# Optimization experiments

Hardware: AMD Instinct MI355X
Metric: run time of the kernel (lower is better)

## Reference

```python
import jax, jax.numpy as jnp
import numpy as np


def setup_inputs() -> dict:
    key = jax.random.key(0)
    ks = jax.random.split(key, 8)
    B, S, P = 512, 128, 32            # batch, seq_len, pred_len
    F, O, H = 64, 64, 1024            # feat_dim, label/output_dim, hidden_dim
    IN = F + O                        # GRUCell input_dim = 128
    w = 0.05                          # weight scale to keep gates in useful range
    return {
        "feats": jax.random.normal(ks[0], (B, S + P - 1, F), jnp.float32),
        "labels": jax.random.normal(ks[1], (B, S, O), jnp.float32),
        "Wi": jax.random.normal(ks[2], (3 * H, IN), jnp.float32) * w,
        "Wh": jax.random.normal(ks[3], (3 * H, H), jnp.float32) * w,
        "bi": jax.random.normal(ks[4], (3 * H,), jnp.float32) * w,
        "bh": jax.random.normal(ks[5], (3 * H,), jnp.float32) * w,
        "Wd": jax.random.normal(ks[6], (O, H), jnp.float32) * w,
        "bd": jax.random.normal(ks[7], (O,), jnp.float32) * w,
    }


def _gru_cell(h, x, Wi, Wh, bi, bh):
    # torch.nn.GRUCell semantics
    gi = x @ Wi.T + bi                       # [B, 3H]
    gh = h @ Wh.T + bh                       # [B, 3H]
    i_r, i_z, i_n = jnp.split(gi, 3, axis=-1)
    h_r, h_z, h_n = jnp.split(gh, 3, axis=-1)
    r = jax.nn.sigmoid(i_r + h_r)
    z = jax.nn.sigmoid(i_z + h_z)
    n = jnp.tanh(i_n + r * h_n)
    return (1.0 - z) * n + z * h


def reference(feats, labels, Wi, Wh, bi, bh, Wd, bd):
    B, S, O = labels.shape
    H = Wh.shape[1]
    prior = feats[:, :S]                     # [B, S, F]
    post = feats[:, S:]                      # [B, P-1, F]
    x = jnp.concatenate([prior, labels], axis=-1)   # [B, S, F+O]

    h0 = jnp.zeros((B, H), feats.dtype)

    def enc_step(h, xt):
        return _gru_cell(h, xt, Wi, Wh, bi, bh), None

    h, _ = jax.lax.scan(enc_step, h0, jnp.swapaxes(x, 0, 1))

    ps = h @ Wd.T + bd                       # decoder output [B, O]

    def dec_step(carry, ft):
        h, ps = carry
        xin = jnp.concatenate([ft, ps], axis=-1)
        h = _gru_cell(h, xin, Wi, Wh, bi, bh)
        ps = h @ Wd.T + bd
        return (h, ps), ps

    _, rest = jax.lax.scan(dec_step, (h, ps), jnp.swapaxes(post, 0, 1))
    return jnp.concatenate([ps[None], rest], axis=0)  # [pred_len, B, O]
```

## Files before the change

### kernel.cpp

```cpp
#include <hip/hip_runtime.h>
#include <cstdint>
#include <cstddef>

#define SENC  128
#define NSTEPS 159
#define HB16  524288
#define XSLICE 131072
#define SLAB_ELEMS 55296
#define FRAG_TOTAL 442368
#define FS 16

typedef short  short8  __attribute__((ext_vector_type(8)));
typedef float  floatx4 __attribute__((ext_vector_type(4)));
typedef float  f32x4   __attribute__((ext_vector_type(4)));
typedef int    i32x4   __attribute__((ext_vector_type(4)));
typedef unsigned long long u64;

#define MFMA(a, b, c) __builtin_amdgcn_mfma_f32_16x16x32_bf16((a), (b), (c), 0, 0, 0)

__device__ __forceinline__ i32x4 ld_nc16(const void* p) {
    i32x4 r;
    asm volatile("global_load_dwordx4 %0, %1, off sc0 sc1" : "=&v"(r) : "v"(p) : "memory");
    return r;
}
__device__ __forceinline__ i32x4 ld_sc0_16(const void* p) {
    i32x4 r;
    asm volatile("global_load_dwordx4 %0, %1, off sc0" : "=&v"(r) : "v"(p) : "memory");
    return r;
}
__device__ __forceinline__ void st_nc8(void* p, u64 v) {
    asm volatile("global_store_dwordx2 %0, %1, off sc0 sc1" :: "v"(p), "v"(v) : "memory");
}
#define WAITVM(N) asm volatile("s_waitcnt vmcnt(" #N ")" ::: "memory")
#define WAITLGKM  asm volatile("s_waitcnt lgkmcnt(0)" ::: "memory")

__device__ __forceinline__ unsigned ldu_dev(const unsigned* p) {
    return __hip_atomic_load(p, __ATOMIC_RELAXED, __HIP_MEMORY_SCOPE_AGENT);
}
__device__ __forceinline__ u64 ldq_dev(const u64* p) {
    return __hip_atomic_load(p, __ATOMIC_RELAXED, __HIP_MEMORY_SCOPE_AGENT);
}
__device__ __forceinline__ void stu_dev(unsigned* p, unsigned v) {
    __hip_atomic_store(p, v, __ATOMIC_RELAXED, __HIP_MEMORY_SCOPE_AGENT);
}
__device__ __forceinline__ void stf_dev(float* p, float v) {
    __hip_atomic_store(p, v, __ATOMIC_RELAXED, __HIP_MEMORY_SCOPE_AGENT);
}

__device__ __forceinline__ unsigned ld_ws(const unsigned* p) {
    return __hip_atomic_load(p, __ATOMIC_RELAXED, __HIP_MEMORY_SCOPE_WORKGROUP);
}
__device__ __forceinline__ void st_ws(unsigned* p, unsigned v) {
    __hip_atomic_store(p, v, __ATOMIC_RELAXED, __HIP_MEMORY_SCOPE_WORKGROUP);
}
__device__ __forceinline__ unsigned add_ws(unsigned* p, unsigned v) {
    return __hip_atomic_fetch_add(p, v, __ATOMIC_RELAXED, __HIP_MEMORY_SCOPE_WORKGROUP);
}

__device__ __forceinline__ float bf2f(short s) {
    return __uint_as_float(((unsigned)(unsigned short)s) << 16);
}
__device__ __forceinline__ short f2bf(float f) {
    unsigned u = __float_as_uint(f);
    return (short)((u + 0x7FFFu + ((u >> 16) & 1u)) >> 16);
}
__device__ __forceinline__ void f2pair(float f, short& hi, short& lo) {
    hi = f2bf(f);
    lo = f2bf(f - bf2f(hi));
}

__device__ __forceinline__ float sigm(float x) {
    return 1.0f / (1.0f + __expf(-x));
}
__device__ __forceinline__ float tanh_fast(float x) {
    float cx = fminf(fmaxf(x, -15.0f), 15.0f);
    float e = __expf(2.0f * cx);
    return (e - 1.0f) / (e + 1.0f);
}

__global__ void setup_swizzle(const float* __restrict__ Wi, const float* __restrict__ Wh,
                              short* __restrict__ whi, short* __restrict__ wlo_x) {
    const int idx = blockIdx.x * 256 + threadIdx.x;
    if (idx >= FRAG_TOTAL) return;
    const int l    = idx & 63;
    const int rest = idx >> 6;
    const int t    = rest % 3;
    const int ki   = (rest / 3) % 36;
    const int c    = rest / 108;
    const int nrow = t * 1024 + c * 16 + (l & 15);
    const int kb   = ki * 32 + (l >> 4) * 8;
    short8 vh, vl;
#pragma unroll
    for (int j = 0; j < 8; ++j) {
        const int k = kb + j;
        float w = (k < 128) ? Wi[(size_t)nrow * 128 + k]
                            : Wh[(size_t)nrow * 1024 + (k - 128)];
        short h, lo2;
        f2pair(w, h, lo2);
        vh[j] = h; vl[j] = lo2;
    }
    *(short8*)(whi + (size_t)idx * 8) = vh;
    if (ki < 4) {
        const int xi = ((c * 4 + ki) * 3 + t) * 64 + l;
        *(short8*)(wlo_x + (size_t)xi * 8) = vl;
    }
}

#define HCONS(S, KI) do { \
    short8 ah_ = *(short8*)&hb[S]; \
    const int fo_ = (((KI) * 3) * 64 + lane) * 8; \
    short8 b0_ = *(const short8*)(s_whi + fo_); \
    short8 b1_ = *(const short8*)(s_whi + fo_ + 512); \
    short8 b2_ = *(const short8*)(s_whi + fo_ + 1024); \
    aR  = MFMA(ah_, b0_, aR); \
    aZ  = MFMA(ah_, b1_, aZ); \
    aNh = MFMA(ah_, b2_, aNh); \
} while (0)

#define IS4(LDFN, B, K0) do { \
    hb[(B) + 0] = LDFN(hrd + ((K0) - 4) * 4096); \
    hb[(B) + 1] = LDFN(hrd + ((K0) - 3) * 4096); \
    hb[(B) + 2] = LDFN(hrd + ((K0) - 2) * 4096); \
    hb[(B) + 3] = LDFN(hrd + ((K0) - 1) * 4096); \
} while (0)

#define CONS4(B, K0) do { \
    HCONS((B) + 0, (K0) + 0); \
    HCONS((B) + 1, (K0) + 1); \
    HCONS((B) + 2, (K0) + 2); \
    HCONS((B) + 3, (K0) + 3); \
} while (0)

#define SPINS(S) do { \
    while (ld_ws(&s_sub[S]) < (unsigned)step) __builtin_amdgcn_s_sleep(2); \
} while (0)

#define REGION2(LDFN) do { \
    i32x4 hb[16]; \
    SPINS(0); IS4(LDFN, 0, 4); \
    SPINS(1); IS4(LDFN, 4, 8); \
    SPINS(2); IS4(LDFN, 8, 12); \
    SPINS(3); IS4(LDFN, 12, 16); \
    WAITVM(12); CONS4(0, 4);   SPINS(4); IS4(LDFN, 0, 20); \
    WAITVM(12); CONS4(4, 8);   SPINS(5); IS4(LDFN, 4, 24); \
    WAITVM(12); CONS4(8, 12);  SPINS(6); IS4(LDFN, 8, 28); \
    WAITVM(12); CONS4(12, 16); SPINS(7); IS4(LDFN, 12, 32); \
    WAITVM(12); CONS4(0, 20); \
    WAITVM(8);  CONS4(4, 24); \
    WAITVM(4);  CONS4(8, 28); \
    WAITVM(0);  CONS4(12, 32); \
} while (0)

#define R1TRIPLE(KI) do { \
    short8 ah_, al_; \
    _Pragma("unroll") \
    for (int j = 0; j < 8; ++j) { short h2_, l2_; f2pair(f[j], h2_, l2_); ah_[j] = h2_; al_[j] = l2_; } \
    const int fo_ = (((KI) * 3) * 64 + lane) * 8; \
    short8 b0_ = *(const short8*)(s_whi + fo_); \
    short8 b1_ = *(const short8*)(s_whi + fo_ + 512); \
    short8 b2_ = *(const short8*)(s_whi + fo_ + 1024); \
    aR  = MFMA(ah_, b0_, aR);  aR  = MFMA(ah_, L0r[KI], aR);  aR  = MFMA(al_, b0_, aR); \
    aZ  = MFMA(ah_, b1_, aZ);  aZ  = MFMA(ah_, L1r[KI], aZ);  aZ  = MFMA(al_, b1_, aZ); \
    aNi = MFMA(ah_, b2_, aNi); aNi = MFMA(ah_, L2r[KI], aNi); aNi = MFMA(al_, b2_, aNi); \
} while (0)

#define LOADF(KI) do { \
    const float* s_ = feats + ((size_t)brow * 159 + step) * 64 + (KI) * 32 + q * 8; \
    f32x4 a_ = ((const f32x4*)s_)[0], b_ = ((const f32x4*)s_)[1]; \
    _Pragma("unroll") for (int j = 0; j < 4; ++j) { f[j] = a_[j]; f[4 + j] = b_[j]; } \
} while (0)

#define LOADL(KI) do { \
    const float* s_ = labels + ((size_t)brow * 128 + step) * 64 + ((KI) - 2) * 32 + q * 8; \
    f32x4 a_ = ((const f32x4*)s_)[0], b_ = ((const f32x4*)s_)[1]; \
    _Pragma("unroll") for (int j = 0; j < 4; ++j) { f[j] = a_[j]; f[4 + j] = b_[j]; } \
} while (0)

#define LOADP(KI) do { \
    const u64* pp_ = (const u64*)(ps_f32 + (size_t)brow * 64 + ((KI) - 2) * 32 + q * 8); \
    _Pragma("unroll") for (int j = 0; j < 4; ++j) { \
        u64 v_ = ldq_dev(pp_ + j); \
        f[2 * j]     = __uint_as_float((unsigned)v_); \
        f[2 * j + 1] = __uint_as_float((unsigned)(v_ >> 32)); } \
} while (0)

__global__ __launch_bounds__(512, 2) void gru_main(
    const float* __restrict__ feats, const float* __restrict__ labels,
    const float* __restrict__ bi,    const float* __restrict__ bh,
    const float* __restrict__ Wd,    const float* __restrict__ bd,
    const short* __restrict__ whi_sw, const short* __restrict__ wlo_x,
    short* __restrict__ h16,         float* __restrict__ ps_f32,
    float* __restrict__ out,
    unsigned* __restrict__ hflag,
    unsigned* __restrict__ pflag,
    int nslots)
{
    __shared__ short s_whi[SLAB_ELEMS];
    __shared__ float s_ps[2048];
    __shared__ short s_tr[8][16][18];
    __shared__ unsigned s_sub[8];
    __shared__ unsigned s_arrD, s_arrI;

    const int tid  = threadIdx.x;
    const int lane = tid & 63;
    const int wv   = tid >> 6;
    const int q    = lane >> 4;
    const int n16  = lane & 15;
    const int c    = blockIdx.x & 63;
    const int r    = blockIdx.x >> 6;
    const bool cached = (nslots > 2);

    if (tid < 8) s_sub[tid] = 0;
    if (tid == 8) s_arrD = 0;
    if (tid == 9) s_arrI = 0;
    {
        const f32x4* src = (const f32x4*)(whi_sw + (size_t)c * SLAB_ELEMS);
        f32x4* dst = (f32x4*)s_whi;
        for (int i = tid; i < SLAB_ELEMS / 8; i += 512) dst[i] = src[i];
    }
    __syncthreads();

    const int mbase = r * 128 + wv * 16;
    const int brow  = mbase + n16;
    const int row_r = c * 16 + n16;
    const float bias_r  = bi[row_r] + bh[row_r];
    const float bias_z  = bi[1024 + row_r] + bh[1024 + row_r];
    const float bias_ni = bi[2048 + row_r];
    const float bias_nh = bh[2048 + row_r];

    unsigned* my_hflag = hflag + (r * 64 + c) * FS;
    unsigned* my_pflag = pflag + (r * 64 + c) * FS;
    const unsigned* hfp     = hflag + (r * 64 + 8 * wv + (lane & 7)) * FS;
    const unsigned* grp_hfl = hflag + (r * 64) * FS;
    const unsigned* grp_pfl = pflag + (r * 64) * FS;

    short8 L0r[4], L1r[4], L2r[4];
#pragma unroll
    for (int ki = 0; ki < 4; ++ki) {
        const short* base = wlo_x + (size_t)(((c * 4 + ki) * 3) * 64 + lane) * 8;
        L0r[ki] = *(const short8*)(base);
        L1r[ki] = *(const short8*)(base + 512);
        L2r[ki] = *(const short8*)(base + 1024);
    }

    float hold[4] = {0.f, 0.f, 0.f, 0.f};

    for (int step = 0; step < NSTEPS; ++step) {
        const bool dec = (step >= SENC);
        const unsigned tgt = (unsigned)(step + 1);
        const int rslot = cached ? step       : (step & 1);
        const int wslot = cached ? (step + 1) : ((step + 1) & 1);
        const short* hrd = h16 + (size_t)rslot * HB16 + (size_t)r * XSLICE
                         + (size_t)(wv * 16 + n16) * 16 + (q & 1) * 8 + (q >> 1) * 2048;
        short* hwr = h16 + (size_t)wslot * HB16 + (size_t)r * XSLICE;

        floatx4 aR  = (floatx4){bias_r,  bias_r,  bias_r,  bias_r};
        floatx4 aZ  = (floatx4){bias_z,  bias_z,  bias_z,  bias_z};
        floatx4 aNi = (floatx4){bias_ni, bias_ni, bias_ni, bias_ni};
        floatx4 aNh = (floatx4){bias_nh, bias_nh, bias_nh, bias_nh};

        {
            float f[8];
            LOADF(0); R1TRIPLE(0);
            LOADF(1); R1TRIPLE(1);

            if (step > 0 && step <= SENC - 1) {
                WAITVM(0);
                if (lane == 0) {
                    unsigned old = add_ws(&s_arrD, 1u);
                    if (old == 8u * (unsigned)step - 1u)
                        stu_dev(my_hflag, (unsigned)step);
                }
            }

            if (!dec) {
                LOADL(2); R1TRIPLE(2);
                LOADL(3); R1TRIPLE(3);
            } else {
                if (wv == 0) {
                    while (ldu_dev(grp_pfl + lane * FS) < (unsigned)step)
                        __builtin_amdgcn_s_sleep(2);
                }
                __syncthreads();
                LOADP(2); R1TRIPLE(2);
                LOADP(3); R1TRIPLE(3);
            }
        }

        if (step > 0) {
            while (!__all(ldu_dev(hfp) >= (unsigned)step))
                __builtin_amdgcn_s_sleep(2);
            if (lane == 0) st_ws(&s_sub[wv], (unsigned)step);
            if (cached) { REGION2(ld_sc0_16); }
            else        { REGION2(ld_nc16); }
        }

        {
#pragma unroll
            for (int i = 0; i < 4; ++i) {
                float rr = sigm(aR[i]);
                float zz = sigm(aZ[i]);
                float nn = tanh_fast(aNi[i] + rr * aNh[i]);
                float hv = (1.0f - zz) * nn + zz * hold[i];
                hold[i] = hv;
                s_tr[wv][q * 4 + i][n16] = f2bf(hv);
            }
            WAITLGKM;
            const int rr2 = lane >> 2, seg = lane & 3;
            u64 v = *(const u64*)&s_tr[wv][rr2][seg * 4];
            st_nc8(hwr + (size_t)c * 2048 + (size_t)(wv * 16 + rr2) * 16 + seg * 4, v);
            if (step >= SENC - 1) {
                WAITVM(0);
                if (lane == 0) {
                    unsigned old = add_ws(&s_arrI, 1u);
                    if (old == 8u * (unsigned)(step - (SENC - 1) + 1) - 1u)
                        stu_dev(my_hflag, tgt);
                }
            }
        }

        if (step >= SENC - 1) {
            const int ot = step - (SENC - 1);
            const int prow0 = r * 128 + 2 * c;
            if (wv == 0) {
                while (ldu_dev(grp_hfl + lane * FS) < tgt)
                    __builtin_amdgcn_s_sleep(2);
            }
            __syncthreads();
            if (tid < 256) {
                const int rl = tid >> 7, rest = tid & 127;
                const int ct = rest >> 1, half = rest & 1;
                const short* src = hwr + (size_t)ct * 2048
                                 + (size_t)(2 * c + rl) * 16 + half * 8;
                i32x4 v = ld_nc16(src);
                WAITVM(0);
                short8 s = *(short8*)&v;
#pragma unroll
                for (int j = 0; j < 8; ++j)
                    s_ps[rl * 1024 + ct * 16 + half * 8 + j] = bf2f(s[j]);
            }
            __syncthreads();
            const int o = tid >> 3, e = tid & 7;
            const float* wrow = Wd + (size_t)o * 1024;
            float acc0 = 0.0f, acc1 = 0.0f;
#pragma unroll 8
            for (int j = 0; j < 32; ++j) {
                const int k = j * 32 + e * 4;
                f32x4 w  = *(const f32x4*)(wrow + k);
                f32x4 a4 = *(const f32x4*)(s_ps + k);
                f32x4 b4 = *(const f32x4*)(s_ps + 1024 + k);
                acc0 += a4[0] * w[0] + a4[1] * w[1] + a4[2] * w[2] + a4[3] * w[3];
                acc1 += b4[0] * w[0] + b4[1] * w[1] + b4[2] * w[2] + b4[3] * w[3];
            }
            acc0 += __shfl_xor(acc0, 1); acc0 += __shfl_xor(acc0, 2); acc0 += __shfl_xor(acc0, 4);
            acc1 += __shfl_xor(acc1, 1); acc1 += __shfl_xor(acc1, 2); acc1 += __shfl_xor(acc1, 4);
            if (e == 0) {
                float v0 = acc0 + bd[o];
                float v1 = acc1 + bd[o];
                out[((size_t)ot * 512 + prow0)     * 64 + o] = v0;
                out[((size_t)ot * 512 + prow0 + 1) * 64 + o] = v1;
                stf_dev(ps_f32 + (size_t)prow0       * 64 + o, v0);
                stf_dev(ps_f32 + (size_t)(prow0 + 1) * 64 + o, v1);
            }
            WAITVM(0);
            __syncthreads();
            if (tid == 0) stu_dev(my_pflag, tgt);
        }
    }
}

extern "C" void kernel_launch(void* const* d_in, const int* in_sizes, int n_in,
                              void* d_out, int out_size, void* d_ws, size_t ws_size,
                              hipStream_t stream) {
    const float* feats  = (const float*)d_in[0];
    const float* labels = (const float*)d_in[1];
    const float* Wi     = (const float*)d_in[2];
    const float* Wh     = (const float*)d_in[3];
    const float* bi     = (const float*)d_in[4];
    const float* bh     = (const float*)d_in[5];
    const float* Wd     = (const float*)d_in[6];
    const float* bd     = (const float*)d_in[7];
    float* out = (float*)d_out;

    char* ws = (char*)d_ws;
    short*    whi_sw = (short*)(ws);
    short*    wlo_x  = (short*)(ws + 7077888);
    float*    ps_f32 = (float*)(ws + 7864320);
    unsigned* pflag  = (unsigned*)(ws + 7995392);
    unsigned* hflag  = (unsigned*)(ws + 8011776);
    short*    h16    = (short*)(ws + 8388608);

    const size_t need = 8388608ull + 160ull * 1048576ull;
    int nslots = (ws_size >= need) ? 160 : 2;

    hipMemsetAsync(ws + 7995392, 0, 32768, stream);

    setup_swizzle<<<FRAG_TOTAL / 256, 256, 0, stream>>>(Wi, Wh, whi_sw, wlo_x);

    void* args[] = {(void*)&feats, (void*)&labels, (void*)&bi, (void*)&bh,
                    (void*)&Wd, (void*)&bd, (void*)&whi_sw, (void*)&wlo_x,
                    (void*)&h16, (void*)&ps_f32, (void*)&out,
                    (void*)&hflag, (void*)&pflag, (void*)&nslots};
    hipLaunchCooperativeKernel(reinterpret_cast<void*>(gru_main),
                               dim3(256), dim3(512), args, 0, stream);
}
```

Measured before the change: 1.483 ms.

## Stagger hidden-state chunk reads per block and publish via atomic swaps

Each block now starts its reads of the shared hidden-state chunks at an offset derived from its column index (c & 7) and wraps around, so that the 64 column blocks do not all spin on and load the same chunk at the same moment. Cross-block stores of the hidden state and the decoder output are changed from plain non-temporal stores and relaxed atomic stores to global atomic swap instructions. The swaps are meant to push the data to the device-coherent level sooner so that consumers polling on other blocks see it with less delay. They add atomic traffic, and the staggered order alters the per-chunk sub-flag wait pattern.

```diff
diff --git a/kernel.cpp b/kernel.cpp
--- a/kernel.cpp
+++ b/kernel.cpp
@@ -28,8 +28,11 @@
     asm volatile("global_load_dwordx4 %0, %1, off sc0" : "=&v"(r) : "v"(p) : "memory");
     return r;
 }
-__device__ __forceinline__ void st_nc8(void* p, u64 v) {
-    asm volatile("global_store_dwordx2 %0, %1, off sc0 sc1" :: "v"(p), "v"(v) : "memory");
+__device__ __forceinline__ void st_swap8(void* p, u64 v) {
+    asm volatile("global_atomic_swap_x2 %0, %1, off sc1" :: "v"(p), "v"(v) : "memory");
+}
+__device__ __forceinline__ void st_swap4(void* p, unsigned v) {
+    asm volatile("global_atomic_swap %0, %1, off sc1" :: "v"(p), "v"(v) : "memory");
 }
 #define WAITVM(N) asm volatile("s_waitcnt vmcnt(" #N ")" ::: "memory")
 #define WAITLGKM  asm volatile("s_waitcnt lgkmcnt(0)" ::: "memory")
@@ -41,9 +44,6 @@
     return __hip_atomic_load(p, __ATOMIC_RELAXED, __HIP_MEMORY_SCOPE_AGENT);
 }
 __device__ __forceinline__ void stu_dev(unsigned* p, unsigned v) {
-    __hip_atomic_store(p, v, __ATOMIC_RELAXED, __HIP_MEMORY_SCOPE_AGENT);
-}
-__device__ __forceinline__ void stf_dev(float* p, float v) {
     __hip_atomic_store(p, v, __ATOMIC_RELAXED, __HIP_MEMORY_SCOPE_AGENT);
 }
 
@@ -117,38 +117,44 @@
     aNh = MFMA(ah_, b2_, aNh); \
 } while (0)
 
-#define IS4(LDFN, B, K0) do { \
-    hb[(B) + 0] = LDFN(hrd + ((K0) - 4) * 4096); \
-    hb[(B) + 1] = LDFN(hrd + ((K0) - 3) * 4096); \
-    hb[(B) + 2] = LDFN(hrd + ((K0) - 2) * 4096); \
-    hb[(B) + 3] = LDFN(hrd + ((K0) - 1) * 4096); \
-} while (0)
-
-#define CONS4(B, K0) do { \
-    HCONS((B) + 0, (K0) + 0); \
-    HCONS((B) + 1, (K0) + 1); \
-    HCONS((B) + 2, (K0) + 2); \
-    HCONS((B) + 3, (K0) + 3); \
-} while (0)
-
-#define SPINS(S) do { \
-    while (ld_ws(&s_sub[S]) < (unsigned)step) __builtin_amdgcn_s_sleep(2); \
+#define CH_ISSUE(LDFN, B, KC) do { \
+    const short* hp_ = hrd + (size_t)(KC) * 16384; \
+    hb[(B) + 0] = LDFN(hp_); \
+    hb[(B) + 1] = LDFN(hp_ + 4096); \
+    hb[(B) + 2] = LDFN(hp_ + 8192); \
+    hb[(B) + 3] = LDFN(hp_ + 12288); \
+} while (0)
+
+#define CH_CONS(B, KC) do { \
+    const int kb_ = 4 + 4 * (KC); \
+    HCONS((B) + 0, kb_ + 0); \
+    HCONS((B) + 1, kb_ + 1); \
+    HCONS((B) + 2, kb_ + 2); \
+    HCONS((B) + 3, kb_ + 3); \
+} while (0)
+
+#define SPIN_CH(KC) do { \
+    while (ld_ws(&s_sub[KC]) < (unsigned)step) __builtin_amdgcn_s_sleep(2); \
 } while (0)
 
 #define REGION2(LDFN) do { \
     i32x4 hb[16]; \
-    SPINS(0); IS4(LDFN, 0, 4); \
-    SPINS(1); IS4(LDFN, 4, 8); \
-    SPINS(2); IS4(LDFN, 8, 12); \
-    SPINS(3); IS4(LDFN, 12, 16); \
-    WAITVM(12); CONS4(0, 4);   SPINS(4); IS4(LDFN, 0, 20); \
-    WAITVM(12); CONS4(4, 8);   SPINS(5); IS4(LDFN, 4, 24); \
-    WAITVM(12); CONS4(8, 12);  SPINS(6); IS4(LDFN, 8, 28); \
-    WAITVM(12); CONS4(12, 16); SPINS(7); IS4(LDFN, 12, 32); \
-    WAITVM(12); CONS4(0, 20); \
-    WAITVM(8);  CONS4(4, 24); \
-    WAITVM(4);  CONS4(8, 28); \
-    WAITVM(0);  CONS4(12, 32); \
+    const int k0_ = r0;            const int k1_ = (r0 + 1) & 7; \
+    const int k2_ = (r0 + 2) & 7;  const int k3_ = (r0 + 3) & 7; \
+    const int k4_ = (r0 + 4) & 7;  const int k5_ = (r0 + 5) & 7; \
+    const int k6_ = (r0 + 6) & 7;  const int k7_ = (r0 + 7) & 7; \
+    SPIN_CH(k0_); CH_ISSUE(LDFN, 0,  k0_); \
+    SPIN_CH(k1_); CH_ISSUE(LDFN, 4,  k1_); \
+    SPIN_CH(k2_); CH_ISSUE(LDFN, 8,  k2_); \
+    SPIN_CH(k3_); CH_ISSUE(LDFN, 12, k3_); \
+    WAITVM(12); CH_CONS(0,  k0_); SPIN_CH(k4_); CH_ISSUE(LDFN, 0,  k4_); \
+    WAITVM(12); CH_CONS(4,  k1_); SPIN_CH(k5_); CH_ISSUE(LDFN, 4,  k5_); \
+    WAITVM(12); CH_CONS(8,  k2_); SPIN_CH(k6_); CH_ISSUE(LDFN, 8,  k6_); \
+    WAITVM(12); CH_CONS(12, k3_); SPIN_CH(k7_); CH_ISSUE(LDFN, 12, k7_); \
+    WAITVM(12); CH_CONS(0,  k4_); \
+    WAITVM(8);  CH_CONS(4,  k5_); \
+    WAITVM(4);  CH_CONS(8,  k6_); \
+    WAITVM(0);  CH_CONS(12, k7_); \
 } while (0)
 
 #define R1TRIPLE(KI) do { \
@@ -208,6 +214,7 @@
     const int n16  = lane & 15;
     const int c    = blockIdx.x & 63;
     const int r    = blockIdx.x >> 6;
+    const int r0   = c & 7;
     const bool cached = (nslots > 2);
 
     if (tid < 8) s_sub[tid] = 0;
@@ -308,7 +315,7 @@
             WAITLGKM;
             const int rr2 = lane >> 2, seg = lane & 3;
             u64 v = *(const u64*)&s_tr[wv][rr2][seg * 4];
-            st_nc8(hwr + (size_t)c * 2048 + (size_t)(wv * 16 + rr2) * 16 + seg * 4, v);
+            st_swap8(hwr + (size_t)c * 2048 + (size_t)(wv * 16 + rr2) * 16 + seg * 4, v);
             if (step >= SENC - 1) {
                 WAITVM(0);
                 if (lane == 0) {
@@ -359,8 +366,8 @@
                 float v1 = acc1 + bd[o];
                 out[((size_t)ot * 512 + prow0)     * 64 + o] = v0;
                 out[((size_t)ot * 512 + prow0 + 1) * 64 + o] = v1;
-                stf_dev(ps_f32 + (size_t)prow0       * 64 + o, v0);
-                stf_dev(ps_f32 + (size_t)(prow0 + 1) * 64 + o, v1);
+                st_swap4(ps_f32 + (size_t)prow0       * 64 + o, __float_as_uint(v0));
+                st_swap4(ps_f32 + (size_t)(prow0 + 1) * 64 + o, __float_as_uint(v1));
             }
             WAITVM(0);
             __syncthreads();
```

New measurement: 1.434 ms. 1.03x faster.
